# Kernel tuning notes

Measured on AMD Instinct MI355X. Metric: run time of the kernel, lower is better.

## Reference

```python
import jax, jax.numpy as jnp
import numpy as np

S = 128      # number of segments
F = 256      # in_features
H = 128      # mlp hidden


def setup_inputs() -> dict:
    key = jax.random.key(0)
    k1, k2, k3 = jax.random.split(key, 3)
    rng = np.random.default_rng(0)
    lengths = rng.integers(1024, 3073, size=S).astype(np.int32)  # ragged segment sizes
    N = int(lengths.sum())  # ~262144 total tokens
    x = jax.random.normal(k1, (N, F), dtype=jnp.float32)
    W1 = jax.random.normal(k2, (F, H), dtype=jnp.float32) * (1.0 / np.sqrt(F))
    b1 = jnp.zeros((H,), dtype=jnp.float32)
    W2 = jax.random.normal(k3, (H, 2), dtype=jnp.float32) * (1.0 / np.sqrt(H))
    b2 = jnp.zeros((2,), dtype=jnp.float32)
    return {"x": x, "lengths": jnp.asarray(lengths), "W1": W1, "b1": b1, "W2": W2, "b2": b2}


def reference(x, lengths, W1, b1, W2, b2):
    N = x.shape[0]
    nseg = lengths.shape[0]
    seg_ids = jnp.repeat(jnp.arange(nseg), lengths, total_repeat_length=N)  # [N]
    offsets = jnp.concatenate([jnp.zeros((1,), lengths.dtype), jnp.cumsum(lengths)[:-1]])
    # position within segment: arange(1, L+1) / L
    pos = (jnp.arange(N) - offsets[seg_ids] + 1).astype(x.dtype)
    Lf = lengths.astype(x.dtype)
    xpos = pos / Lf[seg_ids]  # [N]

    # MLP: Linear -> Tanh -> Linear
    ms = jnp.tanh(x @ W1 + b1) @ W2 + b2  # [N, 2]
    y, z = ms[:, 0], ms[:, 1]

    # per-segment softmax-weighted mean of positions (calc_mean)
    ymax = jax.ops.segment_max(y, seg_ids, num_segments=nseg)
    w = jnp.exp(y - ymax[seg_ids])
    wsum = jax.ops.segment_sum(w, seg_ids, num_segments=nseg)
    means = jax.ops.segment_sum(xpos * w, seg_ids, num_segments=nseg) / wsum  # [S]

    # per-segment softplus(mean(z))
    stds = jax.nn.softplus(jax.ops.segment_sum(z, seg_ids, num_segments=nseg) / Lf)  # [S]

    # normal pdf weights per token
    mu = means[seg_ids]
    sd = stds[seg_ids]
    inv_sqrt_2pi = 1.0 / jnp.sqrt(2.0 * jnp.pi).astype(x.dtype)
    pdf = jnp.exp(-0.5 * ((xpos - mu) / sd) ** 2) * (inv_sqrt_2pi / sd)  # [N]

    # normalize per segment with +0.001 stabilizer
    psum = jax.ops.segment_sum(pdf, seg_ids, num_segments=nseg)
    attn = (pdf / (psum[seg_ids] + 0.001))[:, None]  # [N, 1]

    # attention-weighted sum of features per segment
    out = jax.ops.segment_sum(attn * x, seg_ids, num_segments=nseg)  # [S, F]
    return out, attn
```

## Files before the change

kernel.cpp:

```cpp
#include <hip/hip_runtime.h>
#include <math.h>

#define F 256
#define Hh 128
#define MAXL 3072

typedef short bf16x8 __attribute__((ext_vector_type(8)));
typedef float f32x4 __attribute__((ext_vector_type(4)));
typedef unsigned int uint4v __attribute__((ext_vector_type(4)));

__device__ inline unsigned short f2bf_rne(float f) {
  unsigned u = __float_as_uint(f);
  unsigned r = u + 0x7fff + ((u >> 16) & 1);
  return (unsigned short)(r >> 16);
}
__device__ inline float bf2f(unsigned short h) {
  return __uint_as_float((unsigned)h << 16);
}

__global__ void init_kernel(const int* __restrict__ lengths, int* __restrict__ offsets,
                            float* __restrict__ out, const float* __restrict__ W1,
                            unsigned short* __restrict__ whT, unsigned short* __restrict__ wlT,
                            int S, int outN) {
  int t = blockIdx.x * blockDim.x + threadIdx.x;
  int stride = gridDim.x * blockDim.x;
  for (int i = t; i < outN; i += stride) out[i] = 0.f;
  for (int i = t; i < F * Hh; i += stride) {
    int k = i >> 7, col = i & 127;
    float v = W1[i];
    unsigned short h = f2bf_rne(v);
    unsigned short l = f2bf_rne(v - bf2f(h));
    int dst = (k >> 5) * (128 * 32) + col * 32 + (k & 31);
    whT[dst] = h;
    wlT[dst] = l;
  }
  if (blockIdx.x == 0) {
    __shared__ int buf[256];
    int tid = threadIdx.x;
    int v = (tid < S) ? lengths[tid] : 0;
    buf[tid] = v;
    __syncthreads();
    for (int o = 1; o < 256; o <<= 1) {
      int add = (tid >= o) ? buf[tid - o] : 0;
      __syncthreads();
      buf[tid] += add;
      __syncthreads();
    }
    if (tid < S) offsets[tid] = buf[tid] - v;
    if (tid == S - 1) offsets[S] = buf[tid];
  }
}

__global__ __launch_bounds__(256) void mlp_kernel(
    const float* __restrict__ x,
    const unsigned short* __restrict__ whT, const unsigned short* __restrict__ wlT,
    const float* __restrict__ b1, const float* __restrict__ W2,
    const float* __restrict__ b2, float* __restrict__ yv,
    float* __restrict__ zv, int N) {
  __shared__ float redy[128][2];
  __shared__ float redz[128][2];

  const int t = threadIdx.x;
  const int lane = t & 63;
  const int w = t >> 6;
  const int wr = w >> 1, wc = w & 1;
  const int ln15 = lane & 15, lq = lane >> 4;

  const int row0 = blockIdx.x * 128;

  f32x4 acc[4][4];
#pragma unroll
  for (int i = 0; i < 4; ++i)
#pragma unroll
    for (int j = 0; j < 4; ++j) acc[i][j] = (f32x4){0.f, 0.f, 0.f, 0.f};

  int rowg[4];
  bool rv[4];
#pragma unroll
  for (int rt = 0; rt < 4; ++rt) {
    rowg[rt] = row0 + wr * 64 + rt * 16 + ln15;
    rv[rt] = rowg[rt] < N;
  }
  const int cbase = wc * 64 + ln15;

  for (int kc = 0; kc < 8; ++kc) {
    float4 av0[4], av1[4];
#pragma unroll
    for (int rt = 0; rt < 4; ++rt) {
      av0[rt] = make_float4(0.f, 0.f, 0.f, 0.f);
      av1[rt] = make_float4(0.f, 0.f, 0.f, 0.f);
      if (rv[rt]) {
        const float* p = &x[(size_t)rowg[rt] * F + kc * 32 + lq * 8];
        av0[rt] = *(const float4*)p;
        av1[rt] = *(const float4*)(p + 4);
      }
    }
    bf16x8 bh[4], bl[4];
#pragma unroll
    for (int ct = 0; ct < 4; ++ct) {
      int o = kc * 4096 + (cbase + ct * 16) * 32 + lq * 8;
      bh[ct] = *(const bf16x8*)&whT[o];
      bl[ct] = *(const bf16x8*)&wlT[o];
    }
#pragma unroll
    for (int rt = 0; rt < 4; ++rt) {
      float f[8] = {av0[rt].x, av0[rt].y, av0[rt].z, av0[rt].w,
                    av1[rt].x, av1[rt].y, av1[rt].z, av1[rt].w};
      union { uint4v u; bf16x8 b; } ah, al;
#pragma unroll
      for (int q = 0; q < 4; ++q) {
        unsigned ua = __float_as_uint(f[2 * q]);
        unsigned ub = __float_as_uint(f[2 * q + 1]);
        ah.u[q] = __builtin_amdgcn_perm(ub, ua, 0x07060302u);
        float ra = f[2 * q]     - __uint_as_float(ua & 0xFFFF0000u);
        float rb = f[2 * q + 1] - __uint_as_float(ub & 0xFFFF0000u);
        al.u[q] = __builtin_amdgcn_perm(__float_as_uint(rb), __float_as_uint(ra), 0x07060302u);
      }
#pragma unroll
      for (int ct = 0; ct < 4; ++ct) {
        acc[rt][ct] = __builtin_amdgcn_mfma_f32_16x16x32_bf16(ah.b, bh[ct], acc[rt][ct], 0, 0, 0);
        acc[rt][ct] = __builtin_amdgcn_mfma_f32_16x16x32_bf16(ah.b, bl[ct], acc[rt][ct], 0, 0, 0);
        acc[rt][ct] = __builtin_amdgcn_mfma_f32_16x16x32_bf16(al.b, bh[ct], acc[rt][ct], 0, 0, 0);
      }
    }
  }

  float yp[4][4], zp[4][4];
#pragma unroll
  for (int i = 0; i < 4; ++i)
#pragma unroll
    for (int j = 0; j < 4; ++j) { yp[i][j] = 0.f; zp[i][j] = 0.f; }
#pragma unroll
  for (int ct = 0; ct < 4; ++ct) {
    int c = cbase + ct * 16;
    float b1c = b1[c], wyc = W2[2 * c], wzc = W2[2 * c + 1];
#pragma unroll
    for (int rt = 0; rt < 4; ++rt)
#pragma unroll
      for (int rg = 0; rg < 4; ++rg) {
        float a = acc[rt][ct][rg] + b1c;
        float e = __expf(2.f * a);
        float h = 1.f - __fdividef(2.f, e + 1.f);
        yp[rt][rg] = fmaf(h, wyc, yp[rt][rg]);
        zp[rt][rg] = fmaf(h, wzc, zp[rt][rg]);
      }
  }
#pragma unroll
  for (int rt = 0; rt < 4; ++rt)
#pragma unroll
    for (int rg = 0; rg < 4; ++rg) {
      float vy = yp[rt][rg], vz = zp[rt][rg];
#pragma unroll
      for (int m = 8; m; m >>= 1) {
        vy += __shfl_xor(vy, m);
        vz += __shfl_xor(vz, m);
      }
      if (ln15 == 0) {
        int row = wr * 64 + rt * 16 + lq * 4 + rg;
        redy[row][wc] = vy;
        redz[row][wc] = vz;
      }
    }
  __syncthreads();
  if (t < 128) {
    int g = row0 + t;
    if (g < N) {
      yv[g] = redy[t][0] + redy[t][1] + b2[0];
      zv[g] = redz[t][0] + redz[t][1] + b2[1];
    }
  }
}

__device__ inline float wave_reduce_sum(float v) {
#pragma unroll
  for (int o = 32; o; o >>= 1) v += __shfl_down(v, o);
  return v;
}
__device__ inline float wave_reduce_max(float v) {
#pragma unroll
  for (int o = 32; o; o >>= 1) v = fmaxf(v, __shfl_down(v, o));
  return v;
}

__global__ __launch_bounds__(1024) void stats_kernel(
    const float* __restrict__ yv, const float* __restrict__ zv,
    const int* __restrict__ offsets, const int* __restrict__ lengths,
    float* __restrict__ attn) {
  __shared__ float ybuf[MAXL];
  __shared__ float zbuf[MAXL];
  __shared__ float redA[16], redB[16], redC[16];
  const int s = blockIdx.x;
  const int off = offsets[s];
  const int L = lengths[s];
  const int t = threadIdx.x;
  const int lane = t & 63, wid = t >> 6;

  float lmax = -1e30f;
  for (int i = t; i < L; i += 1024) {
    float yy = yv[off + i];
    ybuf[i] = yy;
    zbuf[i] = zv[off + i];
    lmax = fmaxf(lmax, yy);
  }
  lmax = wave_reduce_max(lmax);
  if (lane == 0) redA[wid] = lmax;
  __syncthreads();
  float ymax = redA[0];
#pragma unroll
  for (int q = 1; q < 16; ++q) ymax = fmaxf(ymax, redA[q]);
  const float invL = 1.f / (float)L;
  __syncthreads();

  float sw = 0.f, smx = 0.f, sz = 0.f;
  for (int i = t; i < L; i += 1024) {
    float wgt = __expf(ybuf[i] - ymax);
    float xp = (float)(i + 1) * invL;
    sw += wgt;
    smx = fmaf(xp, wgt, smx);
    sz += zbuf[i];
  }
  sw = wave_reduce_sum(sw);
  smx = wave_reduce_sum(smx);
  sz = wave_reduce_sum(sz);
  if (lane == 0) { redA[wid] = sw; redB[wid] = smx; redC[wid] = sz; }
  __syncthreads();
  float wsum = 0.f, mxs = 0.f, zsum = 0.f;
#pragma unroll
  for (int q = 0; q < 16; ++q) { wsum += redA[q]; mxs += redB[q]; zsum += redC[q]; }
  const float mu = mxs / wsum;
  const float tz = zsum * invL;
  const float sd = fmaxf(tz, 0.f) + log1pf(__expf(-fabsf(tz)));
  const float invsd = 1.f / sd;
  const float C = 0.3989422804014327f;
  __syncthreads();

  float ps = 0.f;
  for (int i = t; i < L; i += 1024) {
    float xp = (float)(i + 1) * invL;
    float u = (xp - mu) * invsd;
    float p = __expf(-0.5f * u * u) * (C * invsd);
    ybuf[i] = p;
    ps += p;
  }
  ps = wave_reduce_sum(ps);
  if (lane == 0) redA[wid] = ps;
  __syncthreads();
  float psum = 0.f;
#pragma unroll
  for (int q = 0; q < 16; ++q) psum += redA[q];
  const float sc = 1.f / (psum + 0.001f);
  for (int i = t; i < L; i += 1024) attn[off + i] = ybuf[i] * sc;
}

__global__ __launch_bounds__(256) void pool_kernel(
    const float* __restrict__ x, const float* __restrict__ attn,
    const int* __restrict__ offsets, const int* __restrict__ lengths,
    float* __restrict__ out, int nchunks, int S) {
  __shared__ float4 sbuf[4][64];
  const int s = S - 1 - blockIdx.y;
  const int c = nchunks - 1 - blockIdx.x;
  const int off = offsets[s], L = lengths[s];
  const int i0 = (int)((long long)L * c / nchunks);
  const int i1 = (int)((long long)L * (c + 1) / nchunks);
  const int t = threadIdx.x;
  const int lane = t & 63, wid = t >> 6;

  float4 a0 = make_float4(0.f, 0.f, 0.f, 0.f);
  float4 a1 = make_float4(0.f, 0.f, 0.f, 0.f);
  int i = i1 - 1 - wid;
  for (; i - 4 >= i0; i -= 8) {
    float w0 = attn[off + i];
    float w1 = attn[off + i - 4];
    float4 v0 = *(const float4*)&x[(size_t)(off + i) * F + lane * 4];
    float4 v1 = *(const float4*)&x[(size_t)(off + i - 4) * F + lane * 4];
    a0.x = fmaf(w0, v0.x, a0.x); a0.y = fmaf(w0, v0.y, a0.y);
    a0.z = fmaf(w0, v0.z, a0.z); a0.w = fmaf(w0, v0.w, a0.w);
    a1.x = fmaf(w1, v1.x, a1.x); a1.y = fmaf(w1, v1.y, a1.y);
    a1.z = fmaf(w1, v1.z, a1.z); a1.w = fmaf(w1, v1.w, a1.w);
  }
  if (i >= i0) {
    float w0 = attn[off + i];
    float4 v0 = *(const float4*)&x[(size_t)(off + i) * F + lane * 4];
    a0.x = fmaf(w0, v0.x, a0.x); a0.y = fmaf(w0, v0.y, a0.y);
    a0.z = fmaf(w0, v0.z, a0.z); a0.w = fmaf(w0, v0.w, a0.w);
  }
  a0.x += a1.x; a0.y += a1.y; a0.z += a1.z; a0.w += a1.w;
  sbuf[wid][lane] = a0;
  __syncthreads();
  if (wid == 0) {
    float4 r0 = sbuf[0][lane], r1 = sbuf[1][lane];
    float4 r2 = sbuf[2][lane], r3 = sbuf[3][lane];
    float rx = (r0.x + r1.x) + (r2.x + r3.x);
    float ry = (r0.y + r1.y) + (r2.y + r3.y);
    float rz = (r0.z + r1.z) + (r2.z + r3.z);
    float rw = (r0.w + r1.w) + (r2.w + r3.w);
    float* o = &out[s * F + lane * 4];
    atomicAdd(o + 0, rx);
    atomicAdd(o + 1, ry);
    atomicAdd(o + 2, rz);
    atomicAdd(o + 3, rw);
  }
}

extern "C" void kernel_launch(void* const* d_in, const int* in_sizes, int n_in,
                              void* d_out, int out_size, void* d_ws, size_t ws_size,
                              hipStream_t stream) {
  const float* x      = (const float*)d_in[0];
  const int* lengths  = (const int*)d_in[1];
  const float* W1     = (const float*)d_in[2];
  const float* b1     = (const float*)d_in[3];
  const float* W2     = (const float*)d_in[4];
  const float* b2     = (const float*)d_in[5];
  const int S = in_sizes[1];
  const int N = in_sizes[0] / F;

  float* out  = (float*)d_out;
  float* attn = out + (size_t)S * F;

  int*   offsets = (int*)d_ws;
  float* yv = (float*)d_ws + 512;
  float* zv = yv + N;
  unsigned short* whT = (unsigned short*)(zv + N);
  unsigned short* wlT = whT + F * Hh;

  init_kernel<<<64, 256, 0, stream>>>(lengths, offsets, out, W1, whT, wlT, S, S * F);
  mlp_kernel<<<(N + 127) / 128, 256, 0, stream>>>(x, whT, wlT, b1, W2, b2, yv, zv, N);
  stats_kernel<<<S, 1024, 0, stream>>>(yv, zv, offsets, lengths, attn);
  pool_kernel<<<dim3(32, S), 256, 0, stream>>>(x, attn, offsets, lengths, out, 32, S);
}
```

Baseline: 453.7 us.

## Fuse segment stats into pool kernel, recomputing stats redundantly per chunk

Removes the separate per-segment stats kernel. Each of the 32 pool blocks per segment now recomputes the segment's max, weight sums, z mean and pdf sum itself, then writes its slice of attn and computes the weights inline instead of reading attn. This drops one kernel launch and the round trip of attn through memory, but multiplies the stats work (reading y and z and the exp passes) by 32 per segment and grows shared memory use per block.

```diff
diff --git a/kernel.cpp b/kernel.cpp
--- a/kernel.cpp
+++ b/kernel.cpp
@@ -182,95 +182,88 @@
   return v;
 }
 
-__global__ __launch_bounds__(1024) void stats_kernel(
+__global__ __launch_bounds__(256) void pool_kernel(
+    const float* __restrict__ x,
     const float* __restrict__ yv, const float* __restrict__ zv,
     const int* __restrict__ offsets, const int* __restrict__ lengths,
-    float* __restrict__ attn) {
+    float* __restrict__ attn, float* __restrict__ out,
+    int nchunks, int S) {
   __shared__ float ybuf[MAXL];
-  __shared__ float zbuf[MAXL];
-  __shared__ float redA[16], redB[16], redC[16];
-  const int s = blockIdx.x;
-  const int off = offsets[s];
-  const int L = lengths[s];
+  __shared__ float4 sbuf[4][64];
+  __shared__ float redA[4], redB[4], redC[4];
+
+  const int s = S - 1 - blockIdx.y;
+  const int c = nchunks - 1 - blockIdx.x;
+  const int off = offsets[s], L = lengths[s];
   const int t = threadIdx.x;
   const int lane = t & 63, wid = t >> 6;
 
   float lmax = -1e30f;
-  for (int i = t; i < L; i += 1024) {
+  for (int i = t; i < L; i += 256) {
     float yy = yv[off + i];
     ybuf[i] = yy;
-    zbuf[i] = zv[off + i];
     lmax = fmaxf(lmax, yy);
   }
   lmax = wave_reduce_max(lmax);
   if (lane == 0) redA[wid] = lmax;
   __syncthreads();
-  float ymax = redA[0];
-#pragma unroll
-  for (int q = 1; q < 16; ++q) ymax = fmaxf(ymax, redA[q]);
+  const float ymax = fmaxf(fmaxf(redA[0], redA[1]), fmaxf(redA[2], redA[3]));
   const float invL = 1.f / (float)L;
   __syncthreads();
 
   float sw = 0.f, smx = 0.f, sz = 0.f;
-  for (int i = t; i < L; i += 1024) {
+  for (int i = t; i < L; i += 256) {
     float wgt = __expf(ybuf[i] - ymax);
     float xp = (float)(i + 1) * invL;
     sw += wgt;
     smx = fmaf(xp, wgt, smx);
-    sz += zbuf[i];
+    sz += zv[off + i];
   }
   sw = wave_reduce_sum(sw);
   smx = wave_reduce_sum(smx);
   sz = wave_reduce_sum(sz);
   if (lane == 0) { redA[wid] = sw; redB[wid] = smx; redC[wid] = sz; }
   __syncthreads();
-  float wsum = 0.f, mxs = 0.f, zsum = 0.f;
-#pragma unroll
-  for (int q = 0; q < 16; ++q) { wsum += redA[q]; mxs += redB[q]; zsum += redC[q]; }
+  const float wsum = (redA[0] + redA[1]) + (redA[2] + redA[3]);
+  const float mxs  = (redB[0] + redB[1]) + (redB[2] + redB[3]);
+  const float zsum = (redC[0] + redC[1]) + (redC[2] + redC[3]);
   const float mu = mxs / wsum;
   const float tz = zsum * invL;
   const float sd = fmaxf(tz, 0.f) + log1pf(__expf(-fabsf(tz)));
   const float invsd = 1.f / sd;
-  const float C = 0.3989422804014327f;
+  const float Cg = 0.3989422804014327f;
   __syncthreads();
 
   float ps = 0.f;
-  for (int i = t; i < L; i += 1024) {
+  for (int i = t; i < L; i += 256) {
     float xp = (float)(i + 1) * invL;
     float u = (xp - mu) * invsd;
-    float p = __expf(-0.5f * u * u) * (C * invsd);
-    ybuf[i] = p;
-    ps += p;
+    ps += __expf(-0.5f * u * u);
   }
   ps = wave_reduce_sum(ps);
   if (lane == 0) redA[wid] = ps;
   __syncthreads();
-  float psum = 0.f;
-#pragma unroll
-  for (int q = 0; q < 16; ++q) psum += redA[q];
-  const float sc = 1.f / (psum + 0.001f);
-  for (int i = t; i < L; i += 1024) attn[off + i] = ybuf[i] * sc;
-}
-
-__global__ __launch_bounds__(256) void pool_kernel(
-    const float* __restrict__ x, const float* __restrict__ attn,
-    const int* __restrict__ offsets, const int* __restrict__ lengths,
-    float* __restrict__ out, int nchunks, int S) {
-  __shared__ float4 sbuf[4][64];
-  const int s = S - 1 - blockIdx.y;
-  const int c = nchunks - 1 - blockIdx.x;
-  const int off = offsets[s], L = lengths[s];
+  const float psum = ((redA[0] + redA[1]) + (redA[2] + redA[3])) * (Cg * invsd);
+  const float scale = (Cg * invsd) / (psum + 0.001f);
+
   const int i0 = (int)((long long)L * c / nchunks);
   const int i1 = (int)((long long)L * (c + 1) / nchunks);
-  const int t = threadIdx.x;
-  const int lane = t & 63, wid = t >> 6;
+  for (int i = i0 + t; i < i1; i += 256) {
+    float xp = (float)(i + 1) * invL;
+    float u = (xp - mu) * invsd;
+    attn[off + i] = __expf(-0.5f * u * u) * scale;
+  }
 
   float4 a0 = make_float4(0.f, 0.f, 0.f, 0.f);
   float4 a1 = make_float4(0.f, 0.f, 0.f, 0.f);
   int i = i1 - 1 - wid;
   for (; i - 4 >= i0; i -= 8) {
-    float w0 = attn[off + i];
-    float w1 = attn[off + i - 4];
+    float xpa = (float)(i + 1) * invL;
+    float ua = (xpa - mu) * invsd;
+    float w0 = __expf(-0.5f * ua * ua) * scale;
+    float xpb = (float)(i - 3) * invL;
+    float ub = (xpb - mu) * invsd;
+    float w1 = __expf(-0.5f * ub * ub) * scale;
     float4 v0 = *(const float4*)&x[(size_t)(off + i) * F + lane * 4];
     float4 v1 = *(const float4*)&x[(size_t)(off + i - 4) * F + lane * 4];
     a0.x = fmaf(w0, v0.x, a0.x); a0.y = fmaf(w0, v0.y, a0.y);
@@ -279,7 +272,9 @@
     a1.z = fmaf(w1, v1.z, a1.z); a1.w = fmaf(w1, v1.w, a1.w);
   }
   if (i >= i0) {
-    float w0 = attn[off + i];
+    float xpa = (float)(i + 1) * invL;
+    float ua = (xpa - mu) * invsd;
+    float w0 = __expf(-0.5f * ua * ua) * scale;
     float4 v0 = *(const float4*)&x[(size_t)(off + i) * F + lane * 4];
     a0.x = fmaf(w0, v0.x, a0.x); a0.y = fmaf(w0, v0.y, a0.y);
     a0.z = fmaf(w0, v0.z, a0.z); a0.w = fmaf(w0, v0.w, a0.w);
@@ -325,6 +320,5 @@
 
   init_kernel<<<64, 256, 0, stream>>>(lengths, offsets, out, W1, whT, wlT, S, S * F);
   mlp_kernel<<<(N + 127) / 128, 256, 0, stream>>>(x, whT, wlT, b1, W2, b2, yv, zv, N);
-  stats_kernel<<<S, 1024, 0, stream>>>(yv, zv, offsets, lengths, attn);
-  pool_kernel<<<dim3(32, S), 256, 0, stream>>>(x, attn, offsets, lengths, out, 32, S);
-}
+  pool_kernel<<<dim3(32, S), 256, 0, stream>>>(x, yv, zv, offsets, lengths, attn, out, 32, S);
+}
```

Measured after the change: 459.9 us. No clear change (+1.4%).
